# Kernel optimization log

Hardware: AMD Instinct MI355X
Metric: run time of the kernel (lower is better)

Reference implementation:

```python
import jax, jax.numpy as jnp
import numpy as np

D_MODEL = 1024
N_HEADS = 16
D_K = D_MODEL // N_HEADS  # 64
N_CLASSES = 32
S_LEN = 16   # synonyms per class
BATCH = 32
T_LEN = 512  # key/value sequence length


def setup_inputs() -> dict:
    key = jax.random.key(0)
    k1, k2, k3, k4, k5, k6 = jax.random.split(key, 6)
    Q = jax.random.normal(k1, (N_CLASSES, S_LEN, D_MODEL), dtype=jnp.float32)
    H = jax.random.normal(k2, (BATCH, T_LEN, D_MODEL), dtype=jnp.float32)
    ql = jax.random.normal(k3, (N_CLASSES, D_MODEL), dtype=jnp.float32)
    # torch Linear weights are (out_features, in_features), init N(0, 0.001)
    WQ_w = 0.001 * jax.random.normal(k4, (D_MODEL, D_MODEL), dtype=jnp.float32)
    WK_w = 0.001 * jax.random.normal(k5, (D_MODEL, D_MODEL), dtype=jnp.float32)
    WV_w = 0.001 * jax.random.normal(k6, (D_MODEL, D_MODEL), dtype=jnp.float32)
    return {"Q": Q, "H": H, "ql": ql, "WQ_w": WQ_w, "WK_w": WK_w, "WV_w": WV_w}


def reference(Q, H, ql, WQ_w, WK_w, WV_w):
    c, s, d = Q.shape
    b, t, _ = H.shape
    nh, dk = N_HEADS, D_K
    # projections (torch Linear: x @ W.T)
    q_s = (Q @ WQ_w.T).reshape(c, s, nh, dk).transpose(0, 2, 1, 3)   # czsh
    k_s = (H @ WK_w.T).reshape(b, t, nh, dk).transpose(0, 2, 1, 3)   # bzth
    Wql = ql @ WV_w.T                                                # ch
    Hh = H.reshape(b, t, nh, dk).transpose(0, 2, 1, 3)               # bzth
    WK = jnp.tanh(k_s)
    K = jnp.tanh(Hh)
    # scores: (b, c, z, s, t)
    scores = jnp.einsum('bzth,czsh->bczst', WK, q_s)
    attn = jax.nn.softmax(scores, axis=-1)
    # context: (b, c, z, s, h)
    context = jnp.einsum('bzth,bczst->bczsh', K, attn)
    # AvgPool3d((1, s, 1)) + squeeze(-2): mean over s -> (b, c, z, h)
    ctx = context.mean(axis=3).reshape(b, c, nh * dk)                # (b, c, d_model)
    output = jnp.einsum('bch,ch->bc', ctx, Wql)
    return output
```

## Files before the change

### kernel.cpp

```cpp
#include <hip/hip_runtime.h>
#include <hip/hip_bf16.h>
#include <math.h>

#define D_MODEL 1024
#define N_HEADS 16
#define D_K 64
#define N_CLASSES 32
#define S_LEN 16
#define BATCH 32
#define T_LEN 512

typedef __bf16 bf16_t;
typedef bf16_t bf16x8 __attribute__((ext_vector_type(8)));
typedef float f32x4 __attribute__((ext_vector_type(4)));
typedef long lx2 __attribute__((ext_vector_type(2)));

__device__ inline unsigned short f2bf(float f) {
    unsigned int u = __float_as_uint(f);
    unsigned int r = (u + 0x7FFFu + ((u >> 16) & 1u)) >> 16;
    return (unsigned short)r;
}
__device__ inline float fast_tanh(float x) {
    float e = __expf(2.0f * x);
    return (e - 1.0f) * __builtin_amdgcn_rcpf(e + 1.0f);
}
__device__ inline float4 fast_tanh4(float4 v) {
    return make_float4(fast_tanh(v.x), fast_tanh(v.y), fast_tanh(v.z), fast_tanh(v.w));
}
__device__ inline float dot4(float4 a, float4 b) {
    return a.x * b.x + a.y * b.y + a.z * b.z + a.w * b.w;
}
__device__ inline float exp2_fast(float x) {
    float r;
    asm("v_exp_f32 %0, %1" : "=v"(r) : "v"(x));
    return r;
}
__device__ inline int pack_fp8x4(float4 v) {
    int p = __builtin_amdgcn_cvt_pk_fp8_f32(v.x, v.y, 0, false);
    p = __builtin_amdgcn_cvt_pk_fp8_f32(v.z, v.w, p, true);
    return p;
}
__device__ inline bf16x8 bf8_from_f32(const float* p) {
    float4 a = *(const float4*)p;
    float4 b = *(const float4*)(p + 4);
    union { bf16x8 v; unsigned short s[8]; } u;
    u.s[0] = f2bf(a.x); u.s[1] = f2bf(a.y); u.s[2] = f2bf(a.z); u.s[3] = f2bf(a.w);
    u.s[4] = f2bf(b.x); u.s[5] = f2bf(b.y); u.s[6] = f2bf(b.z); u.s[7] = f2bf(b.w);
    return u.v;
}

__device__ inline void async16(void* lds, const void* g) {
    __builtin_amdgcn_global_load_lds(
        (const __attribute__((address_space(1))) unsigned int*)g,
        (__attribute__((address_space(3))) unsigned int*)lds, 16, 0, 0);
}

__global__ __launch_bounds__(256) void prep_kernel(
    const float* __restrict__ H, int* __restrict__ Hf8,
    const float* __restrict__ WK, int* __restrict__ WKf8,
    const float4* __restrict__ Q, ushort4* __restrict__ Qb,
    const float4* __restrict__ WQ, ushort4* __restrict__ WQb,
    const float* __restrict__ ql, const float* __restrict__ WV,
    float* __restrict__ wql)
{
    __shared__ __align__(16) char psm[25600];
    const int bid = blockIdx.x;
    const int tid = threadIdx.x;
    if (bid < 256) {
        float4 (*qls)[16] = (float4(*)[16])psm;
        float4 (*WVs)[17] = (float4(*)[17])(psm + 8192);
        const int n0 = (bid & 15) * 64;
        const int k0 = (bid >> 4) * 64;
        for (int i = tid; i < 512; i += 256)
            qls[i >> 4][i & 15] = *(const float4*)(ql + (size_t)(i >> 4) * D_MODEL + k0 + (i & 15) * 4);
        for (int i = tid; i < 1024; i += 256)
            WVs[i >> 4][i & 15] = *(const float4*)(WV + (size_t)(n0 + (i >> 4)) * D_MODEL + k0 + (i & 15) * 4);
        __syncthreads();

        const int n = tid & 63;
        const int c0 = (tid >> 6) * 8;
        float acc[8] = {};
        for (int kq = 0; kq < 16; kq++) {
            const float4 wv = WVs[n][kq];
#pragma unroll
            for (int c = 0; c < 8; c++) acc[c] += dot4(qls[c0 + c][kq], wv);
        }
#pragma unroll
        for (int c = 0; c < 8; c++)
            atomicAdd(&wql[(size_t)(c0 + c) * D_MODEL + n0 + n], acc[c]);
    } else if (bid < 4608) {
        float (*L)[260] = (float(*)[260])psm;
        int j = bid - 256;
        const float* in; int* out; float s; int jj;
        if (j < 4096) { in = H; out = Hf8; s = 1.0f; jj = j; }
        else { in = WK; out = WKf8; s = 512.0f; jj = j - 4096; }
        const int rb = jj >> 2;
        const int kb0 = (jj & 3) * 4;
        const float* base = in + (size_t)rb * 16 * 1024 + kb0 * 64;
#pragma unroll
        for (int it = 0; it < 4; it++) {
            const int idx = it * 256 + tid;
            const int row = idx >> 6;
            const int c0 = (idx & 63) * 4;
            *(float4*)&L[row][c0] = *(const float4*)(base + (size_t)row * 1024 + c0);
        }
        __syncthreads();
        const int quad = tid >> 6;
        const int l16 = (tid >> 2) & 15;
        const int kh = (tid & 3) >> 1;
        const int b0 = (tid & 1) * 4;
        const int klb = kh * 32 + quad * 8 + b0;
        int* outp = out + (size_t)jj * 1024 + tid;
#pragma unroll
        for (int p = 0; p < 4; p++) {
            float4 v = *(const float4*)&L[l16][p * 64 + klb];
            v.x *= s; v.y *= s; v.z *= s; v.w *= s;
            outp[p * 256] = pack_fp8x4(v);
        }
    } else {
        int i = (bid - 4608) * 256 + tid;
        const float4* in; ushort4* out; float s;
        if (i < 131072) { in = Q + i; out = Qb + i; s = 1.4426950408889634f; }
        else { i -= 131072; in = WQ + i; out = WQb + i; s = 1.0f; }
        float4 v = *in;
        ushort4 o;
        o.x = f2bf(v.x * s); o.y = f2bf(v.y * s); o.z = f2bf(v.z * s); o.w = f2bf(v.w * s);
        *out = o;
    }
}

__global__ __launch_bounds__(512) void gemms_kernel(
    const unsigned char* __restrict__ A8, const unsigned char* __restrict__ B8,
    unsigned short* __restrict__ wkt_b,
    const unsigned short* __restrict__ Qb, const unsigned short* __restrict__ WQb,
    unsigned short* __restrict__ qproj_b,
    const float* __restrict__ H, const float* __restrict__ wql,
    float* __restrict__ kv)
{
    __shared__ __align__(16) char smem[49152];
    const int bid = blockIdx.x;
    const int tid = threadIdx.x;
    const int wid = tid >> 6;
    const int lane = tid & 63;
    const int quad = lane >> 4;
    const int l16 = lane & 15;

    if (bid < 512) {
        unsigned char* As = (unsigned char*)smem;
        unsigned char* Bs = (unsigned char*)smem + 32768;
        const int m0 = (bid & 63) * 256;
        const int n0 = (bid >> 6) * 128;
        const int wm = (wid >> 1) * 64;
        const int wn = (wid & 1) * 64;
        const int stA = wm >> 4;
        const int stB = wn >> 4;
        const int sub = tid >> 6;
        const int cl = lane * 16;

        f32x4 acc[4][4] = {};
        const unsigned char* Ab = A8 + ((size_t)(m0 >> 4) * 16) * 1024;
        const unsigned char* Bb = B8 + ((size_t)(n0 >> 4) * 16) * 1024;

        auto stage = [&](int buf, int kb) {
            async16(&As[buf * 16384 + sub * 1024 + cl],       Ab + ((size_t)sub * 16 + kb) * 1024 + cl);
            async16(&As[buf * 16384 + (sub + 8) * 1024 + cl], Ab + ((size_t)(sub + 8) * 16 + kb) * 1024 + cl);
            async16(&Bs[buf * 8192 + sub * 1024 + cl],        Bb + ((size_t)sub * 16 + kb) * 1024 + cl);
        };

        stage(0, 0);
        __syncthreads();
        for (int kb = 0; kb < 16; kb++) {
            const int cur = kb & 1;
            if (kb < 15) stage(cur ^ 1, kb + 1);

            lx2 a8[4], b8[4];
#pragma unroll
            for (int mt = 0; mt < 4; mt++)
                a8[mt] = *(const lx2*)&As[cur * 16384 + (stA + mt) * 1024 + lane * 16];
#pragma unroll
            for (int nt = 0; nt < 4; nt++)
                b8[nt] = *(const lx2*)&Bs[cur * 8192 + (stB + nt) * 1024 + lane * 16];
#pragma unroll
            for (int mt = 0; mt < 4; mt++)
#pragma unroll
                for (int nt = 0; nt < 4; nt++) {
                    acc[mt][nt] = __builtin_amdgcn_mfma_f32_16x16x32_fp8_fp8(
                        a8[mt].x, b8[nt].x, acc[mt][nt], 0, 0, 0);
                    acc[mt][nt] = __builtin_amdgcn_mfma_f32_16x16x32_fp8_fp8(
                        a8[mt].y, b8[nt].y, acc[mt][nt], 0, 0, 0);
                }
            __syncthreads();
        }

#pragma unroll
        for (int mt = 0; mt < 4; mt++)
#pragma unroll
            for (int nt = 0; nt < 4; nt++)
#pragma unroll
                for (int r = 0; r < 4; r++) {
                    const int row = m0 + wm + mt * 16 + quad * 4 + r;
                    const int col = n0 + wn + nt * 16 + l16;
                    wkt_b[(size_t)row * 1024 + col] =
                        f2bf(fast_tanh(acc[mt][nt][r] * (1.0f / 512.0f)));
                }
    } else if (bid < 544) {
        unsigned short* As = (unsigned short*)smem;
        unsigned short* Bs = (unsigned short*)(smem + 8192);
        const int q = bid - 512;
        const int m0 = (q & 3) * 128;
        const int n0 = (q >> 2) * 128;
        const int wm = (wid >> 1) * 64;
        const int wn = (wid & 1) * 64;

        f32x4 acc[4][4] = {};
        const int r0 = tid >> 2;
        const int cc0 = (tid & 3) * 8;

        for (int k0 = 0; k0 < 1024; k0 += 32) {
            if (tid < 256) {
                async16(&As[tid * 8],        Qb  + (size_t)(m0 + r0) * 1024 + k0 + cc0);
                async16(&As[2048 + tid * 8], Qb  + (size_t)(m0 + 64 + r0) * 1024 + k0 + cc0);
                async16(&Bs[tid * 8],        WQb + (size_t)(n0 + r0) * 1024 + k0 + cc0);
                async16(&Bs[2048 + tid * 8], WQb + (size_t)(n0 + 64 + r0) * 1024 + k0 + cc0);
            }
            __syncthreads();
            if (tid < 256) {
                bf16x8 af[4], bfr[4];
#pragma unroll
                for (int mt = 0; mt < 4; mt++)
                    af[mt] = *(const bf16x8*)&As[(wm + mt * 16 + l16) * 32 + quad * 8];
#pragma unroll
                for (int nt = 0; nt < 4; nt++)
                    bfr[nt] = *(const bf16x8*)&Bs[(wn + nt * 16 + l16) * 32 + quad * 8];
#pragma unroll
                for (int mt = 0; mt < 4; mt++)
#pragma unroll
                    for (int nt = 0; nt < 4; nt++)
                        acc[mt][nt] = __builtin_amdgcn_mfma_f32_16x16x32_bf16(
                            af[mt], bfr[nt], acc[mt][nt], 0, 0, 0);
            }
            __syncthreads();
        }

        if (tid < 256) {
#pragma unroll
            for (int mt = 0; mt < 4; mt++)
#pragma unroll
                for (int nt = 0; nt < 4; nt++)
#pragma unroll
                    for (int r = 0; r < 4; r++) {
                        const int row = m0 + wm + mt * 16 + quad * 4 + r;
                        const int col = n0 + wn + nt * 16 + l16;
                        qproj_b[(size_t)row * 1024 + col] = f2bf(acc[mt][nt][r]);
                    }
        }
    } else {
        unsigned short* Ks = (unsigned short*)smem;
        float* kvt = (float*)(smem + 16384);
        const int q = bid - 544;
        const int chunk = q & 127;
        const int z = q >> 7;
        const int b = chunk >> 2;
        const int t0 = (chunk & 3) * 128;

#pragma unroll
        for (int it = 0; it < 4; it++) {
            const int idx = it * 512 + tid;
            const int row = idx >> 4;
            const int c4 = (idx & 15) * 4;
            float4 v = *(const float4*)(H + ((size_t)b * T_LEN + t0 + row) * D_MODEL + z * D_K + c4);
            v = fast_tanh4(v);
            ushort4 o;
            o.x = f2bf(v.x); o.y = f2bf(v.y); o.z = f2bf(v.z); o.w = f2bf(v.w);
            *(ushort4*)&Ks[row * 64 + c4] = o;
        }
        bf16x8 bfr[2][2];
#pragma unroll
        for (int ct = 0; ct < 2; ct++)
#pragma unroll
            for (int kh = 0; kh < 2; kh++)
                bfr[ct][kh] = bf8_from_f32(wql +
                    (size_t)(ct * 16 + l16) * D_MODEL + z * D_K + kh * 32 + quad * 8);
        __syncthreads();

        const int wt = wid * 16;
        f32x4 acc[2] = {};
        {
            const bf16x8 a0 = *(const bf16x8*)&Ks[(wt + l16) * 64 + quad * 8];
            const bf16x8 a1 = *(const bf16x8*)&Ks[(wt + l16) * 64 + 32 + quad * 8];
#pragma unroll
            for (int ct = 0; ct < 2; ct++) {
                acc[ct] = __builtin_amdgcn_mfma_f32_16x16x32_bf16(a0, bfr[ct][0], acc[ct], 0, 0, 0);
                acc[ct] = __builtin_amdgcn_mfma_f32_16x16x32_bf16(a1, bfr[ct][1], acc[ct], 0, 0, 0);
            }
        }
#pragma unroll
        for (int ct = 0; ct < 2; ct++)
#pragma unroll
            for (int r = 0; r < 4; r++)
                kvt[(wt + quad * 4 + r) * 33 + ct * 16 + l16] = acc[ct][r];
        __syncthreads();

        float* outb = kv + (((size_t)b * 16 + z) * 32) * 512 + t0;
#pragma unroll
        for (int it = 0; it < 2; it++) {
            const int idx = it * 512 + tid;
            const int c = idx >> 5;
            const int tq = (idx & 31) * 4;
            float4 v = make_float4(kvt[(tq + 0) * 33 + c], kvt[(tq + 1) * 33 + c],
                                   kvt[(tq + 2) * 33 + c], kvt[(tq + 3) * 33 + c]);
            *(float4*)(outb + (size_t)c * 512 + tq) = v;
        }
    }
}

__global__ __launch_bounds__(512, 4) void attn_mfma(
    const unsigned short* __restrict__ qproj, const unsigned short* __restrict__ wkt,
    const float* __restrict__ kv, float* __restrict__ part)
{
    __shared__ unsigned short wkts[512 * 64];
    const int z = blockIdx.x;
    const int b = blockIdx.y;
    const int tid = threadIdx.x;
    const int wid = tid >> 6;
    const int lane = tid & 63;
    const int quad = lane >> 4;
    const int l16 = lane & 15;

    const unsigned short* wb = wkt + (size_t)(b * T_LEN) * D_MODEL + z * D_K;
#pragma unroll
    for (int it = 0; it < 8; it++) {
        const int chunk = it * 512 + tid;
        const int row = chunk >> 3;
        const int c = chunk & 7;
        async16(&wkts[chunk * 8], wb + (size_t)row * D_MODEL + ((c ^ (row & 7)) * 8));
    }

    bf16x8 af[4][2];
#pragma unroll
    for (int ct = 0; ct < 4; ct++)
#pragma unroll
        for (int kh = 0; kh < 2; kh++)
            af[ct][kh] = *(const bf16x8*)(qproj +
                (size_t)((wid * 4 + ct) * 16 + l16) * D_MODEL + z * D_K + kh * 32 + quad * 8);
    __syncthreads();

    float den[4][4], num[4][4];
#pragma unroll
    for (int ct = 0; ct < 4; ct++)
#pragma unroll
        for (int r = 0; r < 4; r++) { den[ct][r] = 0.f; num[ct][r] = 0.f; }

    const float* kvp = kv + (((size_t)b * 16 + z) * 32 + wid * 4) * 512 + l16;
    float kc[4], kn[4];
#pragma unroll
    for (int ct = 0; ct < 4; ct++) kc[ct] = kvp[ct * 512];

    const int x0 = (quad ^ (l16 & 7)) * 8;
    const int x1 = ((quad ^ 4) ^ (l16 & 7)) * 8;

    f32x4 a4A[4], a4B[4];
    {
        const int rbase = l16 * 64;
        const bf16x8 b0 = *(const bf16x8*)&wkts[rbase + x0];
        const bf16x8 b1 = *(const bf16x8*)&wkts[rbase + x1];
        __builtin_amdgcn_s_setprio(1);
#pragma unroll
        for (int ct = 0; ct < 4; ct++) {
            f32x4 a = {};
            a = __builtin_amdgcn_mfma_f32_16x16x32_bf16(af[ct][0], b0, a, 0, 0, 0);
            a = __builtin_amdgcn_mfma_f32_16x16x32_bf16(af[ct][1], b1, a, 0, 0, 0);
            a4A[ct] = a;
        }
        __builtin_amdgcn_s_setprio(0);
    }

    for (int nt = 0; nt < 32; nt += 2) {
        {
            const int rb1 = ((nt + 1) * 16 + l16) * 64;
            const bf16x8 c0 = *(const bf16x8*)&wkts[rb1 + x0];
            const bf16x8 c1 = *(const bf16x8*)&wkts[rb1 + x1];
#pragma unroll
            for (int ct = 0; ct < 4; ct++) kn[ct] = kvp[ct * 512 + (nt + 1) * 16];
#pragma unroll
            for (int ct = 0; ct < 4; ct++)
#pragma unroll
                for (int r = 0; r < 4; r++) {
                    const float e = exp2_fast(a4A[ct][r]);
                    den[ct][r] += e;
                    num[ct][r] += e * kc[ct];
                }
            __builtin_amdgcn_s_setprio(1);
#pragma unroll
            for (int ct = 0; ct < 4; ct++) {
                f32x4 a = {};
                a = __builtin_amdgcn_mfma_f32_16x16x32_bf16(af[ct][0], c0, a, 0, 0, 0);
                a = __builtin_amdgcn_mfma_f32_16x16x32_bf16(af[ct][1], c1, a, 0, 0, 0);
                a4B[ct] = a;
            }
            __builtin_amdgcn_s_setprio(0);
#pragma unroll
            for (int ct = 0; ct < 4; ct++) kc[ct] = kn[ct];
        }
        {
            const bool more = (nt + 2) < 32;
            bf16x8 d0 = {}, d1 = {};
            if (more) {
                const int rb2 = ((nt + 2) * 16 + l16) * 64;
                d0 = *(const bf16x8*)&wkts[rb2 + x0];
                d1 = *(const bf16x8*)&wkts[rb2 + x1];
            }
#pragma unroll
            for (int ct = 0; ct < 4; ct++) kn[ct] = kvp[ct * 512 + (nt + 2) * 16];
#pragma unroll
            for (int ct = 0; ct < 4; ct++)
#pragma unroll
                for (int r = 0; r < 4; r++) {
                    const float e = exp2_fast(a4B[ct][r]);
                    den[ct][r] += e;
                    num[ct][r] += e * kc[ct];
                }
            if (more) {
                __builtin_amdgcn_s_setprio(1);
#pragma unroll
                for (int ct = 0; ct < 4; ct++) {
                    f32x4 a = {};
                    a = __builtin_amdgcn_mfma_f32_16x16x32_bf16(af[ct][0], d0, a, 0, 0, 0);
                    a = __builtin_amdgcn_mfma_f32_16x16x32_bf16(af[ct][1], d1, a, 0, 0, 0);
                    a4A[ct] = a;
                }
                __builtin_amdgcn_s_setprio(0);
            }
#pragma unroll
            for (int ct = 0; ct < 4; ct++) kc[ct] = kn[ct];
        }
    }

#pragma unroll
    for (int ct = 0; ct < 4; ct++) {
        float s = 0.f;
#pragma unroll
        for (int r = 0; r < 4; r++) {
            float d = den[ct][r], n = num[ct][r];
#pragma unroll
            for (int off = 1; off < 16; off <<= 1) {
                d += __shfl_xor(d, off, 64);
                n += __shfl_xor(n, off, 64);
            }
            s += n / d;
        }
        s += __shfl_xor(s, 16, 64);
        s += __shfl_xor(s, 32, 64);
        if (lane == 0)
            part[((size_t)(b * N_CLASSES) + wid * 4 + ct) * 16 + z] = s;
    }
}

__global__ __launch_bounds__(256) void attn_reduce(
    const float* __restrict__ part, float* __restrict__ out)
{
    const int i = blockIdx.x * 256 + threadIdx.x;
    const float* p = part + (size_t)i * 16;
    float s = 0.f;
#pragma unroll
    for (int zz = 0; zz < 16; zz++) s += p[zz];
    out[i] = s * (1.0f / 16.0f);
}

extern "C" void kernel_launch(void* const* d_in, const int* in_sizes, int n_in,
                              void* d_out, int out_size, void* d_ws, size_t ws_size,
                              hipStream_t stream)
{
    const float* Q  = (const float*)d_in[0];
    const float* H  = (const float*)d_in[1];
    const float* ql = (const float*)d_in[2];
    const float* WQ = (const float*)d_in[3];
    const float* WK = (const float*)d_in[4];
    const float* WV = (const float*)d_in[5];
    float* out = (float*)d_out;

    char* ws = (char*)d_ws;
    unsigned char*  Hf8     = (unsigned char*)(ws);
    unsigned short* Qb      = (unsigned short*)(ws + (size_t)25165824);
    unsigned short* WQb     = (unsigned short*)(ws + (size_t)26214400);
    unsigned short* qproj_b = (unsigned short*)(ws + (size_t)28311552);
    float*          part    = (float*)(ws + (size_t)30408704);
    float*          wqlb    = (float*)(ws + (size_t)31457280);
    unsigned short* wkt_b   = (unsigned short*)(ws + (size_t)33554432);
    float*          kv      = (float*)(ws + (size_t)67108864);
    unsigned char*  WKf8    = (unsigned char*)(ws + (size_t)100663296);

    dim3 thr(256);
    hipMemsetAsync(wqlb, 0, (size_t)N_CLASSES * D_MODEL * sizeof(float), stream);
    prep_kernel<<<dim3(6144), thr, 0, stream>>>(
        H, (int*)Hf8, WK, (int*)WKf8,
        (const float4*)Q, (ushort4*)Qb,
        (const float4*)WQ, (ushort4*)WQb,
        ql, WV, wqlb);
    gemms_kernel<<<dim3(2592), dim3(512), 0, stream>>>(
        Hf8, WKf8, wkt_b, Qb, WQb, qproj_b, H, wqlb, kv);
    attn_mfma<<<dim3(16, 32), dim3(512), 0, stream>>>(qproj_b, wkt_b, kv, part);
    attn_reduce<<<dim3(4), thr, 0, stream>>>(part, out);
}
```

Before: 206.7 us.

## Shrink gemms_kernel to 256-thread blocks with 128x128 FP8 tiles and finer waitcnt sync

Restructures the fused GEMM kernel to launch 256-thread blocks. The FP8 H·WK GEMM tile shrinks from 256x128 to 128x128, which doubles its block count and halves its shared memory. The double-buffer pipeline now uses explicit vmcnt waits and raw s_barrier instead of __syncthreads, so the next stage's loads can stay in flight. The bf16 Q-projection branch no longer idles half its threads, and the kv branch processes two tiles per wave. The aim is better occupancy and load balance, at the cost of more A/B tile reloads and fragile hand-written sync ordering.

```diff
diff --git a/kernel.cpp b/kernel.cpp
--- a/kernel.cpp
+++ b/kernel.cpp
@@ -129,7 +129,7 @@
     }
 }
 
-__global__ __launch_bounds__(512) void gemms_kernel(
+__global__ __launch_bounds__(256) void gemms_kernel(
     const unsigned char* __restrict__ A8, const unsigned char* __restrict__ B8,
     unsigned short* __restrict__ wkt_b,
     const unsigned short* __restrict__ Qb, const unsigned short* __restrict__ WQb,
@@ -137,7 +137,7 @@
     const float* __restrict__ H, const float* __restrict__ wql,
     float* __restrict__ kv)
 {
-    __shared__ __align__(16) char smem[49152];
+    __shared__ __align__(16) char smem[33280];
     const int bid = blockIdx.x;
     const int tid = threadIdx.x;
     const int wid = tid >> 6;
@@ -145,16 +145,16 @@
     const int quad = lane >> 4;
     const int l16 = lane & 15;
 
-    if (bid < 512) {
+    if (bid < 1024) {
         unsigned char* As = (unsigned char*)smem;
-        unsigned char* Bs = (unsigned char*)smem + 32768;
-        const int m0 = (bid & 63) * 256;
-        const int n0 = (bid >> 6) * 128;
+        unsigned char* Bs = (unsigned char*)smem + 16384;
+        const int m0 = (bid & 127) * 128;
+        const int n0 = (bid >> 7) * 128;
         const int wm = (wid >> 1) * 64;
         const int wn = (wid & 1) * 64;
         const int stA = wm >> 4;
         const int stB = wn >> 4;
-        const int sub = tid >> 6;
+        const int st = wid;
         const int cl = lane * 16;
 
         f32x4 acc[4][4] = {};
@@ -162,21 +162,29 @@
         const unsigned char* Bb = B8 + ((size_t)(n0 >> 4) * 16) * 1024;
 
         auto stage = [&](int buf, int kb) {
-            async16(&As[buf * 16384 + sub * 1024 + cl],       Ab + ((size_t)sub * 16 + kb) * 1024 + cl);
-            async16(&As[buf * 16384 + (sub + 8) * 1024 + cl], Ab + ((size_t)(sub + 8) * 16 + kb) * 1024 + cl);
-            async16(&Bs[buf * 8192 + sub * 1024 + cl],        Bb + ((size_t)sub * 16 + kb) * 1024 + cl);
+            async16(&As[buf * 8192 + tid * 16],        Ab + ((size_t)st * 16 + kb) * 1024 + cl);
+            async16(&As[buf * 8192 + 4096 + tid * 16], Ab + ((size_t)(st + 4) * 16 + kb) * 1024 + cl);
+            async16(&Bs[buf * 8192 + tid * 16],        Bb + ((size_t)st * 16 + kb) * 1024 + cl);
+            async16(&Bs[buf * 8192 + 4096 + tid * 16], Bb + ((size_t)(st + 4) * 16 + kb) * 1024 + cl);
         };
 
         stage(0, 0);
-        __syncthreads();
+        asm volatile("s_waitcnt vmcnt(0)" ::: "memory");
+        __builtin_amdgcn_s_barrier();
         for (int kb = 0; kb < 16; kb++) {
             const int cur = kb & 1;
-            if (kb < 15) stage(cur ^ 1, kb + 1);
+            if (kb < 15) {
+                stage(cur ^ 1, kb + 1);
+                asm volatile("s_waitcnt vmcnt(4)" ::: "memory");
+            } else {
+                asm volatile("s_waitcnt vmcnt(0)" ::: "memory");
+            }
+            __builtin_amdgcn_s_barrier();
 
             lx2 a8[4], b8[4];
 #pragma unroll
             for (int mt = 0; mt < 4; mt++)
-                a8[mt] = *(const lx2*)&As[cur * 16384 + (stA + mt) * 1024 + lane * 16];
+                a8[mt] = *(const lx2*)&As[cur * 8192 + (stA + mt) * 1024 + lane * 16];
 #pragma unroll
             for (int nt = 0; nt < 4; nt++)
                 b8[nt] = *(const lx2*)&Bs[cur * 8192 + (stB + nt) * 1024 + lane * 16];
@@ -189,7 +197,9 @@
                     acc[mt][nt] = __builtin_amdgcn_mfma_f32_16x16x32_fp8_fp8(
                         a8[mt].y, b8[nt].y, acc[mt][nt], 0, 0, 0);
                 }
-            __syncthreads();
+            asm volatile("s_waitcnt lgkmcnt(0)" ::: "memory");
+            __builtin_amdgcn_sched_barrier(0);
+            __builtin_amdgcn_s_barrier();
         }
 
 #pragma unroll
@@ -203,10 +213,10 @@
                     wkt_b[(size_t)row * 1024 + col] =
                         f2bf(fast_tanh(acc[mt][nt][r] * (1.0f / 512.0f)));
                 }
-    } else if (bid < 544) {
+    } else if (bid < 1056) {
         unsigned short* As = (unsigned short*)smem;
         unsigned short* Bs = (unsigned short*)(smem + 8192);
-        const int q = bid - 512;
+        const int q = bid - 1024;
         const int m0 = (q & 3) * 128;
         const int n0 = (q >> 2) * 128;
         const int wm = (wid >> 1) * 64;
@@ -217,55 +227,50 @@
         const int cc0 = (tid & 3) * 8;
 
         for (int k0 = 0; k0 < 1024; k0 += 32) {
-            if (tid < 256) {
-                async16(&As[tid * 8],        Qb  + (size_t)(m0 + r0) * 1024 + k0 + cc0);
-                async16(&As[2048 + tid * 8], Qb  + (size_t)(m0 + 64 + r0) * 1024 + k0 + cc0);
-                async16(&Bs[tid * 8],        WQb + (size_t)(n0 + r0) * 1024 + k0 + cc0);
-                async16(&Bs[2048 + tid * 8], WQb + (size_t)(n0 + 64 + r0) * 1024 + k0 + cc0);
-            }
+            async16(&As[tid * 8],        Qb  + (size_t)(m0 + r0) * 1024 + k0 + cc0);
+            async16(&As[2048 + tid * 8], Qb  + (size_t)(m0 + 64 + r0) * 1024 + k0 + cc0);
+            async16(&Bs[tid * 8],        WQb + (size_t)(n0 + r0) * 1024 + k0 + cc0);
+            async16(&Bs[2048 + tid * 8], WQb + (size_t)(n0 + 64 + r0) * 1024 + k0 + cc0);
             __syncthreads();
-            if (tid < 256) {
-                bf16x8 af[4], bfr[4];
-#pragma unroll
-                for (int mt = 0; mt < 4; mt++)
-                    af[mt] = *(const bf16x8*)&As[(wm + mt * 16 + l16) * 32 + quad * 8];
+
+            bf16x8 af[4], bfr[4];
+#pragma unroll
+            for (int mt = 0; mt < 4; mt++)
+                af[mt] = *(const bf16x8*)&As[(wm + mt * 16 + l16) * 32 + quad * 8];
+#pragma unroll
+            for (int nt = 0; nt < 4; nt++)
+                bfr[nt] = *(const bf16x8*)&Bs[(wn + nt * 16 + l16) * 32 + quad * 8];
+#pragma unroll
+            for (int mt = 0; mt < 4; mt++)
 #pragma unroll
                 for (int nt = 0; nt < 4; nt++)
-                    bfr[nt] = *(const bf16x8*)&Bs[(wn + nt * 16 + l16) * 32 + quad * 8];
-#pragma unroll
-                for (int mt = 0; mt < 4; mt++)
-#pragma unroll
-                    for (int nt = 0; nt < 4; nt++)
-                        acc[mt][nt] = __builtin_amdgcn_mfma_f32_16x16x32_bf16(
-                            af[mt], bfr[nt], acc[mt][nt], 0, 0, 0);
-            }
+                    acc[mt][nt] = __builtin_amdgcn_mfma_f32_16x16x32_bf16(
+                        af[mt], bfr[nt], acc[mt][nt], 0, 0, 0);
             __syncthreads();
         }
 
-        if (tid < 256) {
-#pragma unroll
-            for (int mt = 0; mt < 4; mt++)
-#pragma unroll
-                for (int nt = 0; nt < 4; nt++)
-#pragma unroll
-                    for (int r = 0; r < 4; r++) {
-                        const int row = m0 + wm + mt * 16 + quad * 4 + r;
-                        const int col = n0 + wn + nt * 16 + l16;
-                        qproj_b[(size_t)row * 1024 + col] = f2bf(acc[mt][nt][r]);
-                    }
-        }
+#pragma unroll
+        for (int mt = 0; mt < 4; mt++)
+#pragma unroll
+            for (int nt = 0; nt < 4; nt++)
+#pragma unroll
+                for (int r = 0; r < 4; r++) {
+                    const int row = m0 + wm + mt * 16 + quad * 4 + r;
+                    const int col = n0 + wn + nt * 16 + l16;
+                    qproj_b[(size_t)row * 1024 + col] = f2bf(acc[mt][nt][r]);
+                }
     } else {
         unsigned short* Ks = (unsigned short*)smem;
         float* kvt = (float*)(smem + 16384);
-        const int q = bid - 544;
+        const int q = bid - 1056;
         const int chunk = q & 127;
         const int z = q >> 7;
         const int b = chunk >> 2;
         const int t0 = (chunk & 3) * 128;
 
 #pragma unroll
-        for (int it = 0; it < 4; it++) {
-            const int idx = it * 512 + tid;
+        for (int it = 0; it < 8; it++) {
+            const int idx = it * 256 + tid;
             const int row = idx >> 4;
             const int c4 = (idx & 15) * 4;
             float4 v = *(const float4*)(H + ((size_t)b * T_LEN + t0 + row) * D_MODEL + z * D_K + c4);
@@ -283,28 +288,31 @@
                     (size_t)(ct * 16 + l16) * D_MODEL + z * D_K + kh * 32 + quad * 8);
         __syncthreads();
 
-        const int wt = wid * 16;
-        f32x4 acc[2] = {};
-        {
-            const bf16x8 a0 = *(const bf16x8*)&Ks[(wt + l16) * 64 + quad * 8];
-            const bf16x8 a1 = *(const bf16x8*)&Ks[(wt + l16) * 64 + 32 + quad * 8];
+        const int wt = wid * 32;
+        f32x4 acc[2][2] = {};
+#pragma unroll
+        for (int tt = 0; tt < 2; tt++) {
+            const bf16x8 a0 = *(const bf16x8*)&Ks[(wt + tt * 16 + l16) * 64 + quad * 8];
+            const bf16x8 a1 = *(const bf16x8*)&Ks[(wt + tt * 16 + l16) * 64 + 32 + quad * 8];
 #pragma unroll
             for (int ct = 0; ct < 2; ct++) {
-                acc[ct] = __builtin_amdgcn_mfma_f32_16x16x32_bf16(a0, bfr[ct][0], acc[ct], 0, 0, 0);
-                acc[ct] = __builtin_amdgcn_mfma_f32_16x16x32_bf16(a1, bfr[ct][1], acc[ct], 0, 0, 0);
+                acc[tt][ct] = __builtin_amdgcn_mfma_f32_16x16x32_bf16(a0, bfr[ct][0], acc[tt][ct], 0, 0, 0);
+                acc[tt][ct] = __builtin_amdgcn_mfma_f32_16x16x32_bf16(a1, bfr[ct][1], acc[tt][ct], 0, 0, 0);
             }
         }
 #pragma unroll
-        for (int ct = 0; ct < 2; ct++)
-#pragma unroll
-            for (int r = 0; r < 4; r++)
-                kvt[(wt + quad * 4 + r) * 33 + ct * 16 + l16] = acc[ct][r];
+        for (int tt = 0; tt < 2; tt++)
+#pragma unroll
+            for (int ct = 0; ct < 2; ct++)
+#pragma unroll
+                for (int r = 0; r < 4; r++)
+                    kvt[(wt + tt * 16 + quad * 4 + r) * 33 + ct * 16 + l16] = acc[tt][ct][r];
         __syncthreads();
 
         float* outb = kv + (((size_t)b * 16 + z) * 32) * 512 + t0;
 #pragma unroll
-        for (int it = 0; it < 2; it++) {
-            const int idx = it * 512 + tid;
+        for (int it = 0; it < 4; it++) {
+            const int idx = it * 256 + tid;
             const int c = idx >> 5;
             const int tq = (idx & 31) * 4;
             float4 v = make_float4(kvt[(tq + 0) * 33 + c], kvt[(tq + 1) * 33 + c],
@@ -497,7 +505,7 @@
         (const float4*)Q, (ushort4*)Qb,
         (const float4*)WQ, (ushort4*)WQb,
         ql, WV, wqlb);
-    gemms_kernel<<<dim3(2592), dim3(512), 0, stream>>>(
+    gemms_kernel<<<dim3(3104), thr, 0, stream>>>(
         Hf8, WKf8, wkt_b, Qb, WQb, qproj_b, H, wqlb, kv);
     attn_mfma<<<dim3(16, 32), dim3(512), 0, stream>>>(qproj_b, wkt_b, kv, part);
     attn_reduce<<<dim3(4), thr, 0, stream>>>(part, out);
```

After: 197.2 us. 4.6% less time.
